# Kernel tuning notes

Hardware: AMD Instinct MI355X
Metric: run time of the kernel (lower is better)

The kernel has to match this reference:

```python
import jax, jax.numpy as jnp
import numpy as np

K = 16          # k_neighbors
C = 1.0         # Poincare ball curvature
ALPHA = 0.1     # residual blend strength
EPS = 1e-5


def poincare_project(x, c=C):
    # clip points to lie strictly inside the ball of radius 1/sqrt(c)
    norm = jnp.linalg.norm(x, axis=-1, keepdims=True)
    max_norm = (1.0 - EPS) / jnp.sqrt(c)
    scale = jnp.where(norm > max_norm, max_norm / jnp.maximum(norm, EPS), 1.0)
    return x * scale


def poincare_cdist(x, y, c=C):
    # x: [Nq, d], y: [M, d] -> [Nq, M] pairwise Poincare-ball distances
    x2 = jnp.sum(x * x, axis=-1)                       # [Nq]
    y2 = jnp.sum(y * y, axis=-1)                       # [M]
    xy = x @ y.T                                       # [Nq, M]
    sq = jnp.maximum(x2[:, None] + y2[None, :] - 2.0 * xy, 0.0)
    denom = (1.0 - c * x2)[:, None] * (1.0 - c * y2)[None, :]
    arg = 1.0 + 2.0 * c * sq / jnp.maximum(denom, EPS)
    return jnp.arccosh(jnp.maximum(arg, 1.0 + EPS)) / jnp.sqrt(c)


def layernorm(x, g, b):
    mu = jnp.mean(x, axis=-1, keepdims=True)
    var = jnp.var(x, axis=-1, keepdims=True)
    return (x - mu) * jax.lax.rsqrt(var + EPS) * g + b


def setup_inputs() -> dict:
    key = jax.random.key(0)
    ks = jax.random.split(key, 6)
    Nq, H, D, M = 2048, 1024, 256, 65536
    s1 = 1.0 / np.sqrt(H)
    s2 = 1.0 / np.sqrt(D)
    return {
        "hidden": jax.random.normal(ks[0], (Nq, H), jnp.float32),
        "memory": jax.random.normal(ks[1], (M, D), jnp.float32) * 0.1,
        "w1": jax.random.normal(ks[2], (H, D), jnp.float32) * s1,
        "b1": jnp.zeros((D,), jnp.float32),
        "ln_g": jnp.ones((D,), jnp.float32),
        "ln_b": jnp.zeros((D,), jnp.float32),
        "w2": jax.random.normal(ks[3], (D, D), jnp.float32) * s2,
        "b2": jnp.zeros((D,), jnp.float32),
        "wp": jax.random.normal(ks[4], (D, H), jnp.float32) * s2,
        "bp": jnp.zeros((H,), jnp.float32),
    }


def reference(hidden, memory, w1, b1, ln_g, ln_b, w2, b2, wp, bp):
    # query network: Linear -> LayerNorm -> GELU(exact) -> Linear
    q = layernorm(hidden @ w1 + b1, ln_g, ln_b)
    q = jax.nn.gelu(q, approximate=False) @ w2 + b2          # [Nq, D]

    # project query and memory bank onto the Poincare ball
    q_b = poincare_project(q)
    m_b = poincare_project(memory)

    # hyperbolic kNN: full pairwise distances, then top-k smallest
    dist = poincare_cdist(q_b, m_b)                          # [Nq, M]
    neg_topk, idx = jax.lax.top_k(-dist, K)                  # [Nq, K]

    # distance-weighted aggregation of retrieved memories
    w = jax.nn.softmax(neg_topk, axis=-1)                    # softmax(-dist)
    retrieved = jnp.einsum("nk,nkd->nd", w, m_b[idx])        # [Nq, D]

    # project back to hidden space, residual blend
    out = hidden + ALPHA * (retrieved @ wp + bp)             # [Nq, H]
    return out
```

## Files before the change

### kernel.cpp

```cpp
#include <hip/hip_runtime.h>
#include <hip/hip_bf16.h>

typedef unsigned int u32;
typedef unsigned short u16;
typedef unsigned char u8;
typedef __attribute__((ext_vector_type(8))) short short8;
typedef __attribute__((ext_vector_type(4))) float f32x4;
typedef __attribute__((ext_vector_type(4))) int i32x4;
typedef __attribute__((ext_vector_type(8))) int i32x8;

#define EPSV 1e-5f
#define MAXN (1.0f - 1e-5f)
#define THETA 0.17f
#define CAP 512
#define LCAP 2030u

__device__ __forceinline__ u16 f2bf(float f) {
    union { float f; u32 u; } v; v.f = f;
    u32 u = v.u;
    u32 r = (u + 0x7fffu + ((u >> 16) & 1u)) >> 16;
    return (u16)r;
}
__device__ __forceinline__ float bf2f(u16 h) {
    union { u32 u; float f; } v; v.u = ((u32)h) << 16;
    return v.f;
}
__device__ __forceinline__ u32 pk_fp8x4(float a, float b, float c, float d) {
    int v = __builtin_amdgcn_cvt_pk_fp8_f32(a, b, 0, false);
    v = __builtin_amdgcn_cvt_pk_fp8_f32(c, d, v, true);
    return (u32)v;
}
__device__ __forceinline__ u8 f2fp8(float a) {
    return (u8)(__builtin_amdgcn_cvt_pk_fp8_f32(a, a, 0, false) & 0xFF);
}

typedef __attribute__((address_space(1))) const unsigned char gbuf_t;
typedef __attribute__((address_space(3))) unsigned char lbuf_t;
__device__ __forceinline__ void gl2lds16(const void* g, void* l) {
    __builtin_amdgcn_global_load_lds((gbuf_t*)g, (lbuf_t*)l, 16, 0, 0);
}

__global__ __launch_bounds__(256) void k_pre(const float* __restrict__ mem,
                                             u16* __restrict__ mbf,
                                             u8* __restrict__ mbf8,
                                             float* __restrict__ y2m,
                                             u32* __restrict__ cnt,
                                             const float* __restrict__ hidden, u16* __restrict__ hb,
                                             const float* __restrict__ w1, u16* __restrict__ w1t,
                                             const float* __restrict__ w2, u16* __restrict__ w2t,
                                             const float* __restrict__ wp, u16* __restrict__ wpt) {
    __shared__ float ld[64 * 65];
    const int b = blockIdx.x, t = threadIdx.x;
    if (b < 16384) {
        int zi = b * 256 + t;
        if (zi < 2048) cnt[zi] = 0;
        const int row = b * 4 + (t >> 6);
        const int lane = t & 63;
        const float4* p = (const float4*)(mem + (size_t)row * 256);
        float4 v = p[lane];
        float ss = v.x * v.x + v.y * v.y + v.z * v.z + v.w * v.w;
#pragma unroll
        for (int off = 32; off; off >>= 1) ss += __shfl_xor(ss, off);
        float norm = sqrtf(ss);
        float scale = (norm > MAXN) ? MAXN / fmaxf(norm, EPSV) : 1.0f;
        float x0 = v.x * scale, x1 = v.y * scale, x2 = v.z * scale, x3 = v.w * scale;
        ushort4 u;
        u.x = f2bf(x0); u.y = f2bf(x1); u.z = f2bf(x2); u.w = f2bf(x3);
        *(ushort4*)&mbf[(size_t)row * 256 + lane * 4] = u;
        *(u32*)&mbf8[(size_t)row * 256 + lane * 4] = pk_fp8x4(x0, x1, x2, x3);
        if (lane == 0) y2m[row] = ss * scale * scale;
    } else if (b < 18432) {
        int i = (b - 16384) * 256 + t;
        float4 v = ((const float4*)hidden)[i];
        ushort4 u; u.x = f2bf(v.x); u.y = f2bf(v.y); u.z = f2bf(v.z); u.w = f2bf(v.w);
        ((ushort4*)hb)[i] = u;
    } else {
        const float* src; u16* dst; int K, N, tile;
        int bb = b - 18432;
        if (bb < 64)      { src = w1; dst = w1t; K = 1024; N = 256;  tile = bb; }
        else if (bb < 80) { src = w2; dst = w2t; K = 256;  N = 256;  tile = bb - 64; }
        else              { src = wp; dst = wpt; K = 256;  N = 1024; tile = bb - 80; }
        int ntn = N >> 6;
        int tk = (tile / ntn) * 64, tn = (tile - (tile / ntn) * ntn) * 64;
#pragma unroll
        for (int j = 0; j < 16; ++j) {
            int lin = j * 256 + t;
            int r = lin >> 6, c = lin & 63;
            ld[r * 65 + c] = src[(size_t)(tk + r) * N + tn + c];
        }
        __syncthreads();
#pragma unroll
        for (int j = 0; j < 16; ++j) {
            int lin = j * 256 + t;
            int c2 = lin >> 6, r2 = lin & 63;
            dst[(size_t)(tn + c2) * K + tk + r2] = f2bf(ld[r2 * 65 + c2]);
        }
    }
}

__global__ __launch_bounds__(256) void k_qnet(const u16* __restrict__ hb,
                                              const u16* __restrict__ w1t,
                                              const float* __restrict__ b1,
                                              const float* __restrict__ lng,
                                              const float* __restrict__ lnb,
                                              const u16* __restrict__ w2t,
                                              const float* __restrict__ b2,
                                              u8* __restrict__ qb8,
                                              float* __restrict__ x2q) {
    __shared__ float sm[16 * 260];
    __shared__ u16 qs[16 * 264];
    const int t = threadIdx.x;
    const int w = t >> 6, lane = t & 63;
    const int l16 = lane & 15, kq = (lane >> 4) * 8, rbase = (lane >> 4) * 4;
    const int q0 = blockIdx.x * 16;
    f32x4 zero = {0.f, 0.f, 0.f, 0.f};

    {
        f32x4 acc[4] = {zero, zero, zero, zero};
        const u16* ap = hb + (size_t)(q0 + l16) * 1024 + kq;
        for (int k0 = 0; k0 < 1024; k0 += 32) {
            short8 av = *(const short8*)(ap + k0);
#pragma unroll
            for (int ct = 0; ct < 4; ++ct) {
                int n = w * 64 + ct * 16 + l16;
                short8 bv = *(const short8*)&w1t[(size_t)n * 1024 + k0 + kq];
                acc[ct] = __builtin_amdgcn_mfma_f32_16x16x32_bf16(av, bv, acc[ct], 0, 0, 0);
            }
        }
#pragma unroll
        for (int ct = 0; ct < 4; ++ct) {
            int n = w * 64 + ct * 16 + l16;
            float bias = b1[n];
#pragma unroll
            for (int r = 0; r < 4; ++r)
                sm[(rbase + r) * 260 + n] = acc[ct][r] + bias;
        }
    }
    __syncthreads();
    {
        const int row = t >> 4, sub = t & 15;
        float s1 = 0.f, s2 = 0.f;
#pragma unroll
        for (int i = 0; i < 16; ++i) {
            float v = sm[row * 260 + sub + 16 * i];
            s1 += v; s2 += v * v;
        }
#pragma unroll
        for (int off = 8; off; off >>= 1) {
            s1 += __shfl_xor(s1, off, 16);
            s2 += __shfl_xor(s2, off, 16);
        }
        float mu = s1 * (1.0f / 256.0f);
        float var = s2 * (1.0f / 256.0f) - mu * mu;
        float rstd = rsqrtf(var + EPSV);
#pragma unroll
        for (int i = 0; i < 16; ++i) {
            int cc = sub + 16 * i;
            float v = sm[row * 260 + cc];
            float xn = (v - mu) * rstd * lng[cc] + lnb[cc];
            float ge = 0.5f * xn * (1.0f + erff(xn * 0.7071067811865475f));
            qs[row * 264 + cc] = f2bf(ge);
        }
    }
    __syncthreads();
    f32x4 acc2[4] = {zero, zero, zero, zero};
    for (int k0 = 0; k0 < 256; k0 += 32) {
        short8 av = *(const short8*)&qs[l16 * 264 + k0 + kq];
#pragma unroll
        for (int ct = 0; ct < 4; ++ct) {
            int n = w * 64 + ct * 16 + l16;
            short8 bv = *(const short8*)&w2t[(size_t)n * 256 + k0 + kq];
            acc2[ct] = __builtin_amdgcn_mfma_f32_16x16x32_bf16(av, bv, acc2[ct], 0, 0, 0);
        }
    }
    __syncthreads();
#pragma unroll
    for (int ct = 0; ct < 4; ++ct) {
        int n = w * 64 + ct * 16 + l16;
        float bias = b2[n];
#pragma unroll
        for (int r = 0; r < 4; ++r)
            sm[(rbase + r) * 260 + n] = acc2[ct][r] + bias;
    }
    __syncthreads();
    {
        const int row = t >> 4, sub = t & 15;
        float s2 = 0.f;
#pragma unroll
        for (int i = 0; i < 16; ++i) {
            float v = sm[row * 260 + sub + 16 * i];
            s2 += v * v;
        }
#pragma unroll
        for (int off = 8; off; off >>= 1) s2 += __shfl_xor(s2, off, 16);
        float norm = sqrtf(s2);
        float scale = (norm > MAXN) ? MAXN / fmaxf(norm, EPSV) : 1.0f;
        if (sub == 0) x2q[q0 + row] = s2 * scale * scale;
#pragma unroll
        for (int i = 0; i < 16; ++i) {
            int cc = sub + 16 * i;
            qb8[(size_t)(q0 + row) * 256 + cc] = f2fp8(sm[row * 260 + cc] * scale);
        }
    }
}

__global__ __launch_bounds__(512, 2) void k_dist(const u8* __restrict__ qb8,
                                                 const u8* __restrict__ mbf8,
                                                 u32* __restrict__ cnt,
                                                 uint2* __restrict__ cand) {
    __shared__ __align__(16) u8 ring[49152];
    __shared__ uint2 candL[LCAP];
    __shared__ u32 cntL;
    const int b = blockIdx.x;
    const int xcd = b & 7;
    const int idx = b >> 3;
    const int qt = idx >> 1;
    const int mg = xcd * 2 + (idx & 1);
    const int q0 = qt * 128;
    const int m0 = mg * 4096;
    const int t = threadIdx.x;
    const int w = t >> 6, lane = t & 63;
    const int l16 = lane & 15, Q = lane >> 4, rbase = Q * 4;
    const int wq = w >> 2, wn = w & 3;

    if (t == 0) cntL = 0;

#pragma unroll
    for (int j = 0; j < 4; ++j) {
        int s = j * 512 + t;
        int r = s >> 4, p = s & 15;
        int c = p ^ (r & 15);
        gl2lds16(qb8 + (size_t)(q0 + r) * 256 + c * 16, ring + s * 16);
    }
    __syncthreads();

    i32x8 av[4][2];
#pragma unroll
    for (int i = 0; i < 4; ++i) {
        int R = wq * 64 + i * 16 + l16;
        int aoff = R * 256 + (((Q * 2) ^ (R & 15)) << 4);
#pragma unroll
        for (int st = 0; st < 2; ++st) {
            i32x4 lo = *(const i32x4*)(ring + (aoff ^ (st << 7)));
            i32x4 hi = *(const i32x4*)(ring + (aoff ^ (st << 7) ^ 16));
            av[i][st] = __builtin_shufflevector(lo, hi, 0, 1, 2, 3, 4, 5, 6, 7);
        }
    }
    __syncthreads();

    const int rB = t >> 4;
    const int cB = (t & 15) ^ (rB & 15);
    const u8* srcB = mbf8 + (size_t)(m0 + rB) * 256 + cB * 16;
    const int dstB = t * 16;

    gl2lds16(srcB,                ring + dstB);
    gl2lds16(srcB + 8192,         ring + 8192 + dstB);
    gl2lds16(srcB + 16384,        ring + 16384 + dstB);
    gl2lds16(srcB + 16384 + 8192, ring + 16384 + 8192 + dstB);

    const int S = wn * 16 + l16;
    const int boff = S * 256 + (((Q * 2) ^ (S & 15)) << 4);

    f32x4 zero = {0.f, 0.f, 0.f, 0.f};
    int bcur = 0, bnext = 2;
#pragma unroll 1
    for (int mt = 0; mt < 64; ++mt) {
        if (mt < 63) { asm volatile("s_waitcnt vmcnt(2)" ::: "memory"); }
        else         { asm volatile("s_waitcnt vmcnt(0)" ::: "memory"); }
        __builtin_amdgcn_s_barrier();
        asm volatile("" ::: "memory");
        if (mt < 62) {
            const u8* s0 = srcB + (size_t)(mt + 2) * 16384;
            u8* d0 = ring + bnext * 16384 + dstB;
            gl2lds16(s0, d0);
            gl2lds16(s0 + 8192, d0 + 8192);
        }
        const u8* bufp = ring + bcur * 16384;
        f32x4 acc[4] = {zero, zero, zero, zero};
#pragma unroll
        for (int st = 0; st < 2; ++st) {
            i32x4 blo = *(const i32x4*)(bufp + (boff ^ (st << 7)));
            i32x4 bhi = *(const i32x4*)(bufp + (boff ^ (st << 7) ^ 16));
            i32x8 bv = __builtin_shufflevector(blo, bhi, 0, 1, 2, 3, 4, 5, 6, 7);
#pragma unroll
            for (int i = 0; i < 4; ++i)
                acc[i] = __builtin_amdgcn_mfma_scale_f32_16x16x128_f8f6f4(
                    av[i][st], bv, acc[i], 0, 0, 0, 0x7F7F7F7F, 0, 0x7F7F7F7F);
        }
        const u32 mglob = (u32)(m0 + mt * 64 + wn * 16 + l16);
#pragma unroll
        for (int i = 0; i < 4; ++i) {
            const u32 qloc = (u32)(wq * 64 + i * 16 + rbase);
#pragma unroll
            for (int r = 0; r < 4; ++r) {
                float d = acc[i][r];
                if (d > THETA) {
                    u32 pos = atomicAdd(&cntL, 1u);
                    if (pos < LCAP)
                        candL[pos] = make_uint2(((qloc + (u32)r) << 16) | mglob, __float_as_uint(d));
                }
            }
        }
        bcur = (bcur == 2) ? 0 : bcur + 1;
        bnext = (bnext == 2) ? 0 : bnext + 1;
    }

    __syncthreads();
    u32 n = cntL; if (n > LCAP) n = LCAP;
    for (u32 i2 = (u32)t; i2 < n; i2 += 512u) {
        uint2 e = candL[i2];
        int q = q0 + (int)(e.x >> 16);
        u32 pos = atomicAdd(&cnt[q], 1u);
        if (pos < CAP) cand[(size_t)q * CAP + pos] = make_uint2(e.x & 0xFFFFu, e.y);
    }
}

__global__ __launch_bounds__(64, 4) void k_merge(const u32* __restrict__ cnt,
                                                 const uint2* __restrict__ cand,
                                                 const float* __restrict__ x2q,
                                                 const float* __restrict__ y2m,
                                                 const u16* __restrict__ mbf,
                                                 u16* __restrict__ rb) {
    const int q = blockIdx.x;
    const int lane = threadIdx.x;
    int n = (int)cnt[q]; if (n > CAP) n = CAP;
    const float x2 = x2q[q];
    const float dx = 1.0f - x2;
    float rv[8]; u32 mi[8];
#pragma unroll
    for (int j = 0; j < 8; ++j) {
        int idx = lane + 64 * j;
        rv[j] = 3.0e38f; mi[j] = 0;
        if (idx < n) {
            uint2 c = cand[(size_t)q * CAP + idx];
            float dot = __uint_as_float(c.y);
            float y2 = y2m[c.x];
            float sq = fmaxf(x2 + y2 - 2.0f * dot, 0.0f);
            float den = fmaxf(dx * (1.0f - y2), EPSV);
            rv[j] = sq / den;
            mi[j] = c.x;
        }
    }
    __shared__ float sdist[16];
    __shared__ u32 smi[16];
    __shared__ float swt[16];
    for (int k = 0; k < 16; ++k) {
        float lm = rv[0]; int ls = 0;
#pragma unroll
        for (int j = 1; j < 8; ++j) if (rv[j] < lm) { lm = rv[j]; ls = j; }
        unsigned long long key = (((unsigned long long)__float_as_uint(lm)) << 32) | (u32)(lane * 8 + ls);
#pragma unroll
        for (int off = 32; off; off >>= 1) {
            unsigned long long o = __shfl_xor(key, off);
            key = (o < key) ? o : key;
        }
        u32 sid = (u32)(key & 0xffffffffu);
        int wl = (int)(sid >> 3), wslot = (int)(sid & 7);
        if (lane == wl) {
            sdist[k] = rv[wslot];
            smi[k] = mi[wslot];
            rv[wslot] = 3.0e38f;
        }
    }
    __syncthreads();
    float rr = sdist[lane & 15];
    float arg = fmaxf(fmaf(2.0f, rr, 1.0f), 1.0f + EPSV);
    float dneg = -acoshf(arg);
    float mx = dneg;
#pragma unroll
    for (int off = 8; off; off >>= 1) mx = fmaxf(mx, __shfl_xor(mx, off, 16));
    float e = expf(dneg - mx);
    float ssum = e;
#pragma unroll
    for (int off = 8; off; off >>= 1) ssum += __shfl_xor(ssum, off, 16);
    if (lane < 16) swt[lane] = e / ssum;
    __syncthreads();
    float acc[4] = {0.f, 0.f, 0.f, 0.f};
    for (int k = 0; k < 16; ++k) {
        float wk = swt[k];
        const u16* mr = mbf + (size_t)smi[k] * 256;
#pragma unroll
        for (int j = 0; j < 4; ++j) acc[j] += wk * bf2f(mr[lane + 64 * j]);
    }
#pragma unroll
    for (int j = 0; j < 4; ++j) rb[(size_t)q * 256 + lane + 64 * j] = f2bf(acc[j]);
}

__global__ __launch_bounds__(256) void k_out(const u16* __restrict__ rb,
                                             const u16* __restrict__ wpt,
                                             const float* __restrict__ bp,
                                             const float* __restrict__ hidden,
                                             float* __restrict__ out) {
    const int b = blockIdx.x;
    const int mt = b & 31, nt = b >> 5;
    const int t = threadIdx.x;
    const int w = t >> 6, lane = t & 63;
    const int l16 = lane & 15, kq = (lane >> 4) * 8, rbase = (lane >> 4) * 4;
    const int n = nt * 64 + w * 16 + l16;
    f32x4 zero = {0.f, 0.f, 0.f, 0.f};
    f32x4 acc[4] = {zero, zero, zero, zero};
    for (int k0 = 0; k0 < 256; k0 += 32) {
        short8 bv = *(const short8*)&wpt[(size_t)n * 256 + k0 + kq];
#pragma unroll
        for (int rt = 0; rt < 4; ++rt) {
            short8 av = *(const short8*)&rb[(size_t)(mt * 64 + rt * 16 + l16) * 256 + k0 + kq];
            acc[rt] = __builtin_amdgcn_mfma_f32_16x16x32_bf16(av, bv, acc[rt], 0, 0, 0);
        }
    }
    float bpn = bp[n];
#pragma unroll
    for (int rt = 0; rt < 4; ++rt)
#pragma unroll
        for (int r = 0; r < 4; ++r) {
            int m = mt * 64 + rt * 16 + rbase + r;
            out[(size_t)m * 1024 + n] = hidden[(size_t)m * 1024 + n] + 0.1f * (acc[rt][r] + bpn);
        }
}

extern "C" void kernel_launch(void* const* d_in, const int* in_sizes, int n_in,
                              void* d_out, int out_size, void* d_ws, size_t ws_size,
                              hipStream_t stream) {
    const float* hidden = (const float*)d_in[0];
    const float* memory = (const float*)d_in[1];
    const float* w1 = (const float*)d_in[2];
    const float* b1 = (const float*)d_in[3];
    const float* ln_g = (const float*)d_in[4];
    const float* ln_b = (const float*)d_in[5];
    const float* w2 = (const float*)d_in[6];
    const float* b2 = (const float*)d_in[7];
    const float* wp = (const float*)d_in[8];
    const float* bp = (const float*)d_in[9];
    float* out = (float*)d_out;
    char* ws = (char*)d_ws;

    u16* mbf  = (u16*)(ws);
    float* y2m = (float*)(ws + 33554432);
    u16* hb   = (u16*)(ws + 33816576);
    u16* w1t  = (u16*)(ws + 38010880);
    u16* w2t  = (u16*)(ws + 38535168);
    u16* wpt  = (u16*)(ws + 38666240);
    u8*  qb8  = (u8*)(ws + 40239104);
    float* x2q = (float*)(ws + 41287680);
    u32* cnt  = (u32*)(ws + 41295872);
    uint2* cand = (uint2*)(ws + 41304064);
    u16* rb   = (u16*)(ws + 49692672);
    u8*  mbf8 = (u8*)(ws + 50741248);

    hipLaunchKernelGGL(k_pre, dim3(18576), dim3(256), 0, stream,
                       memory, mbf, mbf8, y2m, cnt, hidden, hb, w1, w1t, w2, w2t, wp, wpt);
    hipLaunchKernelGGL(k_qnet, dim3(128), dim3(256), 0, stream,
                       hb, w1t, b1, ln_g, ln_b, w2t, b2, qb8, x2q);
    hipLaunchKernelGGL(k_dist, dim3(256), dim3(512), 0, stream, qb8, mbf8, cnt, cand);
    hipLaunchKernelGGL(k_merge, dim3(2048), dim3(64), 0, stream, cnt, cand, x2q, y2m, mbf, rb);
    hipLaunchKernelGGL(k_out, dim3(512), dim3(256), 0, stream, rb, wpt, bp, hidden, out);
}
```

Baseline: 301.4 us.

## Restructure k_dist into per-wave private rings with ballot-based candidate compaction

The distance kernel now uses 256-thread blocks covering 64 queries each, with twice as many blocks. Each wave owns its own double-buffered LDS slice of memory rows, which removes the block-wide barrier from every tile iteration. The shared LDS atomic counter for threshold candidates is replaced by per-wave ballot/popcount compaction into per-wave buffers, then flushed to global memory. The trade-off is that the query tile loaded into LDS is reused across fewer memory rows, and per-wave candidate buffers may overflow sooner (512 entries each).

```diff
diff --git a/kernel.cpp b/kernel.cpp
--- a/kernel.cpp
+++ b/kernel.cpp
@@ -13,7 +13,7 @@
 #define MAXN (1.0f - 1e-5f)
 #define THETA 0.17f
 #define CAP 512
-#define LCAP 2030u
+#define LCAPW 512u
 
 __device__ __forceinline__ u16 f2bf(float f) {
     union { float f; u32 u; } v; v.f = f;
@@ -204,30 +204,28 @@
     }
 }
 
-__global__ __launch_bounds__(512, 2) void k_dist(const u8* __restrict__ qb8,
+__global__ __launch_bounds__(256, 3) void k_dist(const u8* __restrict__ qb8,
                                                  const u8* __restrict__ mbf8,
                                                  u32* __restrict__ cnt,
                                                  uint2* __restrict__ cand) {
-    __shared__ __align__(16) u8 ring[49152];
-    __shared__ uint2 candL[LCAP];
-    __shared__ u32 cntL;
+    __shared__ __align__(16) u8 ring[32768];
+    __shared__ uint2 candW[4 * LCAPW];
+    __shared__ u32 wcntS[4];
     const int b = blockIdx.x;
     const int xcd = b & 7;
     const int idx = b >> 3;
     const int qt = idx >> 1;
     const int mg = xcd * 2 + (idx & 1);
-    const int q0 = qt * 128;
+    const int q0 = qt * 64;
     const int m0 = mg * 4096;
     const int t = threadIdx.x;
     const int w = t >> 6, lane = t & 63;
     const int l16 = lane & 15, Q = lane >> 4, rbase = Q * 4;
-    const int wq = w >> 2, wn = w & 3;
-
-    if (t == 0) cntL = 0;
+    const int wn = w;
 
 #pragma unroll
     for (int j = 0; j < 4; ++j) {
-        int s = j * 512 + t;
+        int s = j * 256 + t;
         int r = s >> 4, p = s & 15;
         int c = p ^ (r & 15);
         gl2lds16(qb8 + (size_t)(q0 + r) * 256 + c * 16, ring + s * 16);
@@ -237,8 +235,8 @@
     i32x8 av[4][2];
 #pragma unroll
     for (int i = 0; i < 4; ++i) {
-        int R = wq * 64 + i * 16 + l16;
-        int aoff = R * 256 + (((Q * 2) ^ (R & 15)) << 4);
+        int R = i * 16 + l16;
+        int aoff = R * 256 + (((Q * 2) ^ l16) << 4);
 #pragma unroll
         for (int st = 0; st < 2; ++st) {
             i32x4 lo = *(const i32x4*)(ring + (aoff ^ (st << 7)));
@@ -248,70 +246,88 @@
     }
     __syncthreads();
 
-    const int rB = t >> 4;
-    const int cB = (t & 15) ^ (rB & 15);
-    const u8* srcB = mbf8 + (size_t)(m0 + rB) * 256 + cB * 16;
-    const int dstB = t * 16;
-
-    gl2lds16(srcB,                ring + dstB);
-    gl2lds16(srcB + 8192,         ring + 8192 + dstB);
-    gl2lds16(srcB + 16384,        ring + 16384 + dstB);
-    gl2lds16(srcB + 16384 + 8192, ring + 16384 + 8192 + dstB);
-
-    const int S = wn * 16 + l16;
-    const int boff = S * 256 + (((Q * 2) ^ (S & 15)) << 4);
+    const int rl = (lane >> 4);
+    const int pch = lane & 15;
+    const u8* pB[4];
+#pragma unroll
+    for (int i = 0; i < 4; ++i) {
+        int rr = i * 4 + rl;
+        int c = pch ^ rr;
+        pB[i] = mbf8 + (size_t)(m0 + wn * 16 + rr) * 256 + c * 16;
+    }
+    u8* const wring = ring + w * 8192;
+    const int ldst = lane * 16;
+
+#pragma unroll
+    for (int i = 0; i < 4; ++i) gl2lds16(pB[i], wring + i * 1024 + ldst);
+#pragma unroll
+    for (int i = 0; i < 4; ++i) gl2lds16(pB[i] + 16384, wring + 4096 + i * 1024 + ldst);
+
+    const int boff = l16 * 256 + (((Q * 2) ^ l16) << 4);
 
     f32x4 zero = {0.f, 0.f, 0.f, 0.f};
-    int bcur = 0, bnext = 2;
+    u32 wcnt = 0;
+    const u32 mgbase = (u32)(m0 + wn * 16 + l16);
+
 #pragma unroll 1
     for (int mt = 0; mt < 64; ++mt) {
-        if (mt < 63) { asm volatile("s_waitcnt vmcnt(2)" ::: "memory"); }
+        if (mt < 63) { asm volatile("s_waitcnt vmcnt(4)" ::: "memory"); }
         else         { asm volatile("s_waitcnt vmcnt(0)" ::: "memory"); }
-        __builtin_amdgcn_s_barrier();
-        asm volatile("" ::: "memory");
+        const u8* bufp = wring + ((mt & 1) << 12);
+        i32x4 r00 = *(const i32x4*)(bufp + boff);
+        i32x4 r01 = *(const i32x4*)(bufp + (boff ^ 16));
+        i32x4 r10 = *(const i32x4*)(bufp + (boff ^ 128));
+        i32x4 r11 = *(const i32x4*)(bufp + (boff ^ 128 ^ 16));
+        asm volatile("s_waitcnt lgkmcnt(0)" ::: "memory");
+        __builtin_amdgcn_sched_barrier(0);
         if (mt < 62) {
-            const u8* s0 = srcB + (size_t)(mt + 2) * 16384;
-            u8* d0 = ring + bnext * 16384 + dstB;
-            gl2lds16(s0, d0);
-            gl2lds16(s0 + 8192, d0 + 8192);
-        }
-        const u8* bufp = ring + bcur * 16384;
+            const size_t so = (size_t)(mt + 2) * 16384;
+            u8* d = (u8*)bufp;
+#pragma unroll
+            for (int i = 0; i < 4; ++i) gl2lds16(pB[i] + so, d + i * 1024 + ldst);
+        }
+        i32x8 bv0 = __builtin_shufflevector(r00, r01, 0, 1, 2, 3, 4, 5, 6, 7);
+        i32x8 bv1 = __builtin_shufflevector(r10, r11, 0, 1, 2, 3, 4, 5, 6, 7);
         f32x4 acc[4] = {zero, zero, zero, zero};
 #pragma unroll
-        for (int st = 0; st < 2; ++st) {
-            i32x4 blo = *(const i32x4*)(bufp + (boff ^ (st << 7)));
-            i32x4 bhi = *(const i32x4*)(bufp + (boff ^ (st << 7) ^ 16));
-            i32x8 bv = __builtin_shufflevector(blo, bhi, 0, 1, 2, 3, 4, 5, 6, 7);
-#pragma unroll
-            for (int i = 0; i < 4; ++i)
-                acc[i] = __builtin_amdgcn_mfma_scale_f32_16x16x128_f8f6f4(
-                    av[i][st], bv, acc[i], 0, 0, 0, 0x7F7F7F7F, 0, 0x7F7F7F7F);
-        }
-        const u32 mglob = (u32)(m0 + mt * 64 + wn * 16 + l16);
-#pragma unroll
-        for (int i = 0; i < 4; ++i) {
-            const u32 qloc = (u32)(wq * 64 + i * 16 + rbase);
+        for (int i = 0; i < 4; ++i)
+            acc[i] = __builtin_amdgcn_mfma_scale_f32_16x16x128_f8f6f4(
+                av[i][0], bv0, acc[i], 0, 0, 0, 0x7F7F7F7F, 0, 0x7F7F7F7F);
+#pragma unroll
+        for (int i = 0; i < 4; ++i)
+            acc[i] = __builtin_amdgcn_mfma_scale_f32_16x16x128_f8f6f4(
+                av[i][1], bv1, acc[i], 0, 0, 0, 0x7F7F7F7F, 0, 0x7F7F7F7F);
+        const u32 mglob = mgbase + (u32)(mt * 64);
+#pragma unroll
+        for (int i = 0; i < 4; ++i)
 #pragma unroll
             for (int r = 0; r < 4; ++r) {
                 float d = acc[i][r];
-                if (d > THETA) {
-                    u32 pos = atomicAdd(&cntL, 1u);
-                    if (pos < LCAP)
-                        candL[pos] = make_uint2(((qloc + (u32)r) << 16) | mglob, __float_as_uint(d));
+                unsigned long long mask = __ballot(d > THETA);
+                if (mask) {
+                    if (d > THETA) {
+                        u32 pos = wcnt + (u32)__popcll(mask & ((1ull << lane) - 1ull));
+                        if (pos < LCAPW)
+                            candW[w * LCAPW + pos] =
+                                make_uint2(((u32)(i * 16 + rbase + r) << 16) | mglob,
+                                           __float_as_uint(d));
+                    }
+                    wcnt += (u32)__popcll(mask);
                 }
             }
-        }
-        bcur = (bcur == 2) ? 0 : bcur + 1;
-        bnext = (bnext == 2) ? 0 : bnext + 1;
-    }
-
-    __syncthreads();
-    u32 n = cntL; if (n > LCAP) n = LCAP;
-    for (u32 i2 = (u32)t; i2 < n; i2 += 512u) {
-        uint2 e = candL[i2];
-        int q = q0 + (int)(e.x >> 16);
-        u32 pos = atomicAdd(&cnt[q], 1u);
-        if (pos < CAP) cand[(size_t)q * CAP + pos] = make_uint2(e.x & 0xFFFFu, e.y);
+    }
+
+    if (lane == 0) wcntS[w] = wcnt;
+    __syncthreads();
+#pragma unroll 1
+    for (int wv = 0; wv < 4; ++wv) {
+        u32 n = wcntS[wv]; if (n > LCAPW) n = LCAPW;
+        for (u32 i = (u32)t; i < n; i += 256u) {
+            uint2 e = candW[wv * LCAPW + i];
+            int q = q0 + (int)(e.x >> 16);
+            u32 pos = atomicAdd(&cnt[q], 1u);
+            if (pos < CAP) cand[(size_t)q * CAP + pos] = make_uint2(e.x & 0xFFFFu, e.y);
+        }
     }
 }
 
@@ -450,7 +466,7 @@
                        memory, mbf, mbf8, y2m, cnt, hidden, hb, w1, w1t, w2, w2t, wp, wpt);
     hipLaunchKernelGGL(k_qnet, dim3(128), dim3(256), 0, stream,
                        hb, w1t, b1, ln_g, ln_b, w2t, b2, qb8, x2q);
-    hipLaunchKernelGGL(k_dist, dim3(256), dim3(512), 0, stream, qb8, mbf8, cnt, cand);
+    hipLaunchKernelGGL(k_dist, dim3(512), dim3(256), 0, stream, qb8, mbf8, cnt, cand);
     hipLaunchKernelGGL(k_merge, dim3(2048), dim3(64), 0, stream, cnt, cand, x2q, y2m, mbf, rb);
     hipLaunchKernelGGL(k_out, dim3(512), dim3(256), 0, stream, rb, wpt, bp, hidden, out);
 }
```

Result: faster. 272.1 us (-9.7%).
